# Optimization experiments

Hardware: AMD Instinct MI355X
Metric: run time of the kernel (lower is better)

## Reference

```python
import jax, jax.numpy as jnp
import numpy as np

N = 1500
GAT_IN = 32
GAT_OUT = 8
MLP_HIDDEN = 128
ALPHA = 0.2  # leaky relu slope
NEG_INF = -9.0e15


def setup_inputs() -> dict:
    key = jax.random.key(0)
    ks = jax.random.split(key, 16)
    eye = jnp.eye(N, dtype=jnp.float32)
    geo_adj = jnp.maximum((jax.random.uniform(ks[0], (N, N)) < 0.02).astype(jnp.float32), eye)
    sem_adj = jnp.maximum((jax.random.uniform(ks[1], (N, N)) < 0.02).astype(jnp.float32), eye)
    features = jax.random.normal(ks[2], (N, GAT_IN), dtype=jnp.float32)
    # all (i, j) region pairs, as in the original source
    ii, jj = jnp.meshgrid(jnp.arange(N), jnp.arange(N), indexing='ij')
    region_pairs = jnp.stack([ii.reshape(-1), jj.reshape(-1)], axis=1).astype(jnp.int64)
    distance_features = jax.random.uniform(ks[3], (N * N, 1), dtype=jnp.float32)
    def lin(k, fan_in, fan_out):
        return jax.random.normal(k, (fan_in, fan_out), dtype=jnp.float32) / jnp.sqrt(jnp.float32(fan_in))
    W0 = lin(ks[4], GAT_IN, GAT_OUT)
    W1 = lin(ks[5], GAT_OUT, GAT_OUT)
    W2 = lin(ks[6], GAT_OUT, GAT_OUT)
    a0 = lin(ks[7], 2 * GAT_OUT, 1)
    a1 = lin(ks[8], 2 * GAT_OUT, 1)
    a2 = lin(ks[9], 2 * GAT_OUT, 1)
    fc1_w = lin(ks[10], 2 * GAT_OUT + 1, MLP_HIDDEN)
    fc1_b = jnp.zeros((MLP_HIDDEN,), dtype=jnp.float32)
    fc2_w = lin(ks[11], MLP_HIDDEN, 1)
    fc2_b = jnp.zeros((1,), dtype=jnp.float32)
    return {"geo_adj": geo_adj, "sem_adj": sem_adj, "features": features,
            "region_pairs": region_pairs, "distance_features": distance_features,
            "W0": W0, "W1": W1, "W2": W2, "a0": a0, "a1": a1, "a2": a2,
            "fc1_w": fc1_w, "fc1_b": fc1_b, "fc2_w": fc2_w, "fc2_b": fc2_b}


def _gat_layer(combined_adj, feats, W, a):
    # h = W feats; attention score a([h_i || h_j]) decomposes into h_i@a1 + h_j@a2
    h = feats @ W                      # [N, out]
    f_src = h @ a[:GAT_OUT]            # [N, 1]
    f_dst = h @ a[GAT_OUT:]            # [N, 1]
    e = jax.nn.leaky_relu(f_src + f_dst.T, negative_slope=ALPHA)  # [N, N]
    e = e * combined_adj
    att = jax.nn.softmax(jnp.where(combined_adj > 0, e, NEG_INF), axis=1)
    return jax.nn.elu(att @ h)


def reference(geo_adj, sem_adj, features, region_pairs, distance_features,
              W0, W1, W2, a0, a1, a2, fc1_w, fc1_b, fc2_w, fc2_b):
    combined_adj = geo_adj + sem_adj
    enc = features
    for W, a in ((W0, a0), (W1, a1), (W2, a2)):
        enc = _gat_layer(combined_adj, enc, W, a)
    r1 = enc[region_pairs[:, 0]]       # [N^2, out]
    r2 = enc[region_pairs[:, 1]]       # [N^2, out]
    comb = jnp.concatenate([r1, r2, distance_features], axis=1)  # [N^2, 17]
    hid = jax.nn.relu(comb @ fc1_w + fc1_b)
    return hid @ fc2_w + fc2_b
```

## Files before the change

kernel.cpp:

```cpp
#include <hip/hip_runtime.h>
#include <hip/hip_bf16.h>

#define NN 1500
#define GIN 32
#define GOUT 8
#define HID 128
#define CAP 192

typedef float v2f __attribute__((ext_vector_type(2)));

__global__ void build_csr(const float* __restrict__ geo,
                          const float* __restrict__ sem,
                          int* __restrict__ csr_idx,
                          float* __restrict__ csr_val,
                          int* __restrict__ csr_cnt) {
    const int i = blockIdx.x;
    const int t = threadIdx.x;
    __shared__ int cnt;
    __shared__ int sidx[CAP];
    __shared__ float sval[CAP];
    if (t == 0) cnt = 0;
    __syncthreads();
    const float* grow = geo + (size_t)i * NN;
    const float* srow = sem + (size_t)i * NN;
    for (int q = t; q < NN / 4; q += 256) {
        float4 g = *(const float4*)(grow + 4 * q);
        float4 s = *(const float4*)(srow + 4 * q);
        float a[4] = {g.x + s.x, g.y + s.y, g.z + s.z, g.w + s.w};
        #pragma unroll
        for (int c = 0; c < 4; ++c) {
            if (a[c] > 0.f) {
                int p = atomicAdd(&cnt, 1);
                if (p < CAP) { sidx[p] = 4 * q + c; sval[p] = a[c]; }
            }
        }
    }
    __syncthreads();
    int c2 = cnt < CAP ? cnt : CAP;
    if (t == 0) csr_cnt[i] = c2;
    for (int p = t; p < c2; p += 256) {
        csr_idx[(size_t)i * CAP + p] = sidx[p];
        csr_val[(size_t)i * CAP + p] = sval[p];
    }
}

template<int IN>
__global__ void gat_layer(const float* __restrict__ enc,
                          const float* __restrict__ W,
                          const float* __restrict__ avec,
                          const int* __restrict__ csr_idx,
                          const float* __restrict__ csr_val,
                          const int* __restrict__ csr_cnt,
                          float* __restrict__ enc_out) {
    const int tid = threadIdx.x;
    const int lane = tid & 63;
    const int i = blockIdx.x * 4 + (tid >> 6);

    float hv = 0.f;
    if (lane < GOUT) {
        #pragma unroll 4
        for (int c = 0; c < IN; ++c)
            hv = fmaf(enc[(size_t)i * IN + c], W[c * GOUT + lane], hv);
    }
    float hi[GOUT];
    #pragma unroll
    for (int c = 0; c < GOUT; ++c) hi[c] = __shfl(hv, c, 64);
    float fsrc = 0.f;
    #pragma unroll
    for (int c = 0; c < GOUT; ++c) fsrc = fmaf(hi[c], avec[c], fsrc);

    const int cnt = csr_cnt[i];
    float den = 0.f;
    float num[GOUT] = {};
    for (int e = lane; e < cnt; e += 64) {
        int j = csr_idx[(size_t)i * CAP + e];
        float a = csr_val[(size_t)i * CAP + e];
        float hj[GOUT] = {};
        #pragma unroll
        for (int c4 = 0; c4 < IN / 4; ++c4) {
            float4 e4 = *(const float4*)(enc + (size_t)j * IN + 4 * c4);
            const float* ep = (const float*)&e4;
            #pragma unroll
            for (int c = 0; c < 4; ++c)
                #pragma unroll
                for (int k = 0; k < GOUT; ++k)
                    hj[k] = fmaf(ep[c], W[(4 * c4 + c) * GOUT + k], hj[k]);
        }
        float fd = 0.f;
        #pragma unroll
        for (int k = 0; k < GOUT; ++k) fd = fmaf(hj[k], avec[GOUT + k], fd);
        float ev = fsrc + fd;
        ev = (ev > 0.f) ? ev : 0.2f * ev;
        ev *= a;
        float p = __expf(ev);
        den += p;
        #pragma unroll
        for (int k = 0; k < GOUT; ++k) num[k] = fmaf(p, hj[k], num[k]);
    }
    #pragma unroll
    for (int off = 32; off > 0; off >>= 1) {
        den += __shfl_xor(den, off, 64);
        #pragma unroll
        for (int k = 0; k < GOUT; ++k) num[k] += __shfl_xor(num[k], off, 64);
    }
    if (lane < GOUT) {
        float v = num[lane] / den;
        enc_out[(size_t)i * GOUT + lane] = (v > 0.f) ? v : (__expf(v) - 1.f);
    }
}

#define TILE 48
#define STRIDE 132

__global__ __launch_bounds__(256, 3) void mlp_kernel(
        const float* __restrict__ enc,
        const float* __restrict__ dist,
        const float* __restrict__ fc1w,
        const float* __restrict__ fc1b,
        const float* __restrict__ fc2w,
        const float* __restrict__ fc2b,
        float* __restrict__ out) {
    __shared__ float Us[TILE * STRIDE];
    __shared__ float Vs[TILE * STRIDE];
    __shared__ float w16s[HID];
    __shared__ float f2s[HID];

    const int tid = threadIdx.x;
    const int i0 = blockIdx.y * TILE;
    const int j0 = blockIdx.x * TILE;

    {
        const int kg = tid & 31;
        const int k4 = kg << 2;
        const int rb = tid >> 5;
        float4 b4 = *(const float4*)(fc1b + k4);
        for (int r = rb; r < TILE; r += 8) {
            int gi = i0 + r; if (gi >= NN) gi = NN - 1;
            int gj = j0 + r; if (gj >= NN) gj = NN - 1;
            float4 u = b4;
            float4 v = {0.f, 0.f, 0.f, 0.f};
            #pragma unroll
            for (int c = 0; c < GOUT; ++c) {
                float ei = enc[(size_t)gi * GOUT + c];
                float ej = enc[(size_t)gj * GOUT + c];
                float4 wu = *(const float4*)(fc1w + c * HID + k4);
                float4 wv = *(const float4*)(fc1w + (GOUT + c) * HID + k4);
                u.x = fmaf(ei, wu.x, u.x); u.y = fmaf(ei, wu.y, u.y);
                u.z = fmaf(ei, wu.z, u.z); u.w = fmaf(ei, wu.w, u.w);
                v.x = fmaf(ej, wv.x, v.x); v.y = fmaf(ej, wv.y, v.y);
                v.z = fmaf(ej, wv.z, v.z); v.w = fmaf(ej, wv.w, v.w);
            }
            *(float4*)(Us + r * STRIDE + k4) = u;
            *(float4*)(Vs + r * STRIDE + k4) = v;
        }
        if (tid < HID) {
            w16s[tid] = fc1w[2 * GOUT * HID + tid];
            f2s[tid] = fc2w[tid];
        }
    }
    __syncthreads();

    const int tx = tid & 15;
    const int ty = tid >> 4;

    int irow[3], jcol[3];
    float d[3][3];
    #pragma unroll
    for (int ii = 0; ii < 3; ++ii) irow[ii] = i0 + ty + 16 * ii;
    #pragma unroll
    for (int jj = 0; jj < 3; ++jj) jcol[jj] = j0 + tx + 16 * jj;
    #pragma unroll
    for (int ii = 0; ii < 3; ++ii) {
        int ic = irow[ii] < NN ? irow[ii] : NN - 1;
        #pragma unroll
        for (int jj = 0; jj < 3; ++jj) {
            int jc = jcol[jj] < NN ? jcol[jj] : NN - 1;
            d[ii][jj] = dist[(size_t)ic * NN + jc];
        }
    }

    v2f acc[3][3] = {};
    for (int k = 0; k < HID; k += 4) {
        float4 u4[3], v4[3];
        #pragma unroll
        for (int ii = 0; ii < 3; ++ii)
            u4[ii] = *(const float4*)(Us + (ty + 16 * ii) * STRIDE + k);
        #pragma unroll
        for (int jj = 0; jj < 3; ++jj)
            v4[jj] = *(const float4*)(Vs + (tx + 16 * jj) * STRIDE + k);
        float4 wk = *(const float4*)(w16s + k);
        float4 fk = *(const float4*)(f2s + k);
        const v2f* wp = (const v2f*)&wk;
        const v2f* fp = (const v2f*)&fk;
        #pragma unroll
        for (int h = 0; h < 2; ++h) {
            v2f w2 = wp[h];
            v2f f2 = fp[h];
            #pragma unroll
            for (int ii = 0; ii < 3; ++ii) {
                v2f u2 = ((const v2f*)&u4[ii])[h];
                #pragma unroll
                for (int jj = 0; jj < 3; ++jj) {
                    v2f t = u2 + ((const v2f*)&v4[jj])[h];
                    t = t + w2 * d[ii][jj];
                    t = __builtin_elementwise_max(t, (v2f)0.f);
                    acc[ii][jj] = acc[ii][jj] + t * f2;
                }
            }
        }
    }

    const float b2 = fc2b[0];
    #pragma unroll
    for (int ii = 0; ii < 3; ++ii) {
        if (irow[ii] >= NN) continue;
        #pragma unroll
        for (int jj = 0; jj < 3; ++jj) {
            if (jcol[jj] >= NN) continue;
            out[(size_t)irow[ii] * NN + jcol[jj]] = acc[ii][jj].x + acc[ii][jj].y + b2;
        }
    }
}

extern "C" void kernel_launch(void* const* d_in, const int* in_sizes, int n_in,
                              void* d_out, int out_size, void* d_ws, size_t ws_size,
                              hipStream_t stream) {
    const float* geo  = (const float*)d_in[0];
    const float* sem  = (const float*)d_in[1];
    const float* feat = (const float*)d_in[2];
    const float* dist = (const float*)d_in[4];
    const float* W0   = (const float*)d_in[5];
    const float* W1   = (const float*)d_in[6];
    const float* W2   = (const float*)d_in[7];
    const float* a0   = (const float*)d_in[8];
    const float* a1   = (const float*)d_in[9];
    const float* a2   = (const float*)d_in[10];
    const float* fc1w = (const float*)d_in[11];
    const float* fc1b = (const float*)d_in[12];
    const float* fc2w = (const float*)d_in[13];
    const float* fc2b = (const float*)d_in[14];
    float* out = (float*)d_out;

    char* ws = (char*)d_ws;
    int*   csr_idx = (int*)ws;                         ws += sizeof(int) * NN * CAP;
    float* csr_val = (float*)ws;                       ws += sizeof(float) * NN * CAP;
    int*   csr_cnt = (int*)ws;                         ws += sizeof(int) * NN;
    float* encA    = (float*)ws;                       ws += sizeof(float) * NN * GOUT;
    float* encB    = (float*)ws;

    build_csr<<<NN, 256, 0, stream>>>(geo, sem, csr_idx, csr_val, csr_cnt);

    gat_layer<GIN><<<NN / 4, 256, 0, stream>>>(feat, W0, a0, csr_idx, csr_val, csr_cnt, encA);
    gat_layer<GOUT><<<NN / 4, 256, 0, stream>>>(encA, W1, a1, csr_idx, csr_val, csr_cnt, encB);
    gat_layer<GOUT><<<NN / 4, 256, 0, stream>>>(encB, W2, a2, csr_idx, csr_val, csr_cnt, encA);

    dim3 mg((NN + TILE - 1) / TILE, (NN + TILE - 1) / TILE);
    mlp_kernel<<<mg, 256, 0, stream>>>(encA, dist, fc1w, fc1b, fc2w, fc2b, out);
}
```

Before: 160.5 us.

## Fuse first GAT layer into CSR build and enlarge MLP register tile

The CSR-building kernel now also computes the first GAT layer, so one launch and a re-read of the CSR arrays go away. Each thread handles one neighbour and the result is reduced across the block. The pairwise MLP kernel moves from 48x48 tiles with 3x3 outputs per thread to 96x96 tiles with 6x6 outputs per thread. Its hidden dimension is staged through shared memory in two 64-wide phases, which raises register reuse of U/V loads but cuts occupancy to one block per SIMD-bound launch and gives only 256 blocks.

```diff
diff --git a/kernel.cpp b/kernel.cpp
--- a/kernel.cpp
+++ b/kernel.cpp
@@ -9,18 +9,25 @@
 
 typedef float v2f __attribute__((ext_vector_type(2)));
 
-__global__ void build_csr(const float* __restrict__ geo,
+__global__ void gat_first(const float* __restrict__ geo,
                           const float* __restrict__ sem,
+                          const float* __restrict__ feat,
+                          const float* __restrict__ W0,
+                          const float* __restrict__ a0,
                           int* __restrict__ csr_idx,
                           float* __restrict__ csr_val,
-                          int* __restrict__ csr_cnt) {
+                          int* __restrict__ csr_cnt,
+                          float* __restrict__ enc_out) {
     const int i = blockIdx.x;
     const int t = threadIdx.x;
     __shared__ int cnt;
     __shared__ int sidx[CAP];
     __shared__ float sval[CAP];
+    __shared__ float hi_s[GOUT];
+    __shared__ float wsum[4][GOUT + 1];
     if (t == 0) cnt = 0;
     __syncthreads();
+
     const float* grow = geo + (size_t)i * NN;
     const float* srow = sem + (size_t)i * NN;
     for (int q = t; q < NN / 4; q += 256) {
@@ -35,12 +42,68 @@
             }
         }
     }
+    if (t < GOUT) {
+        float hv = 0.f;
+        #pragma unroll 4
+        for (int c = 0; c < GIN; ++c)
+            hv = fmaf(feat[(size_t)i * GIN + c], W0[c * GOUT + t], hv);
+        hi_s[t] = hv;
+    }
     __syncthreads();
-    int c2 = cnt < CAP ? cnt : CAP;
+
+    const int c2 = cnt < CAP ? cnt : CAP;
     if (t == 0) csr_cnt[i] = c2;
     for (int p = t; p < c2; p += 256) {
         csr_idx[(size_t)i * CAP + p] = sidx[p];
         csr_val[(size_t)i * CAP + p] = sval[p];
+    }
+    float fsrc = 0.f;
+    #pragma unroll
+    for (int k = 0; k < GOUT; ++k) fsrc = fmaf(hi_s[k], a0[k], fsrc);
+
+    float den = 0.f;
+    float num[GOUT] = {};
+    if (t < c2) {
+        int j = sidx[t];
+        float a = sval[t];
+        float hj[GOUT] = {};
+        #pragma unroll
+        for (int c4 = 0; c4 < GIN / 4; ++c4) {
+            float4 e4 = *(const float4*)(feat + (size_t)j * GIN + 4 * c4);
+            const float* ep = (const float*)&e4;
+            #pragma unroll
+            for (int c = 0; c < 4; ++c)
+                #pragma unroll
+                for (int k = 0; k < GOUT; ++k)
+                    hj[k] = fmaf(ep[c], W0[(4 * c4 + c) * GOUT + k], hj[k]);
+        }
+        float fd = 0.f;
+        #pragma unroll
+        for (int k = 0; k < GOUT; ++k) fd = fmaf(hj[k], a0[GOUT + k], fd);
+        float ev = fsrc + fd;
+        ev = (ev > 0.f) ? ev : 0.2f * ev;
+        ev *= a;
+        float p = __expf(ev);
+        den = p;
+        #pragma unroll
+        for (int k = 0; k < GOUT; ++k) num[k] = p * hj[k];
+    }
+    #pragma unroll
+    for (int off = 32; off > 0; off >>= 1) {
+        den += __shfl_xor(den, off, 64);
+        #pragma unroll
+        for (int k = 0; k < GOUT; ++k) num[k] += __shfl_xor(num[k], off, 64);
+    }
+    if ((t & 63) == 0) {
+        wsum[t >> 6][0] = den;
+        #pragma unroll
+        for (int k = 0; k < GOUT; ++k) wsum[t >> 6][1 + k] = num[k];
+    }
+    __syncthreads();
+    if (t < GOUT) {
+        float L = wsum[0][0] + wsum[1][0] + wsum[2][0] + wsum[3][0];
+        float v = (wsum[0][1 + t] + wsum[1][1 + t] + wsum[2][1 + t] + wsum[3][1 + t]) / L;
+        enc_out[(size_t)i * GOUT + t] = (v > 0.f) ? v : (__expf(v) - 1.f);
     }
 }
 
@@ -109,10 +172,11 @@
     }
 }
 
-#define TILE 48
-#define STRIDE 132
-
-__global__ __launch_bounds__(256, 3) void mlp_kernel(
+#define MT 96
+#define KS 64
+#define KSTR 68
+
+__global__ __launch_bounds__(256, 1) void mlp_kernel(
         const float* __restrict__ enc,
         const float* __restrict__ dist,
         const float* __restrict__ fc1w,
@@ -120,102 +184,106 @@
         const float* __restrict__ fc2w,
         const float* __restrict__ fc2b,
         float* __restrict__ out) {
-    __shared__ float Us[TILE * STRIDE];
-    __shared__ float Vs[TILE * STRIDE];
+    __shared__ float Us[MT * KSTR];
+    __shared__ float Vs[MT * KSTR];
     __shared__ float w16s[HID];
     __shared__ float f2s[HID];
 
     const int tid = threadIdx.x;
-    const int i0 = blockIdx.y * TILE;
-    const int j0 = blockIdx.x * TILE;
-
-    {
-        const int kg = tid & 31;
-        const int k4 = kg << 2;
-        const int rb = tid >> 5;
-        float4 b4 = *(const float4*)(fc1b + k4);
-        for (int r = rb; r < TILE; r += 8) {
-            int gi = i0 + r; if (gi >= NN) gi = NN - 1;
-            int gj = j0 + r; if (gj >= NN) gj = NN - 1;
-            float4 u = b4;
-            float4 v = {0.f, 0.f, 0.f, 0.f};
-            #pragma unroll
-            for (int c = 0; c < GOUT; ++c) {
-                float ei = enc[(size_t)gi * GOUT + c];
-                float ej = enc[(size_t)gj * GOUT + c];
-                float4 wu = *(const float4*)(fc1w + c * HID + k4);
-                float4 wv = *(const float4*)(fc1w + (GOUT + c) * HID + k4);
-                u.x = fmaf(ei, wu.x, u.x); u.y = fmaf(ei, wu.y, u.y);
-                u.z = fmaf(ei, wu.z, u.z); u.w = fmaf(ei, wu.w, u.w);
-                v.x = fmaf(ej, wv.x, v.x); v.y = fmaf(ej, wv.y, v.y);
-                v.z = fmaf(ej, wv.z, v.z); v.w = fmaf(ej, wv.w, v.w);
-            }
-            *(float4*)(Us + r * STRIDE + k4) = u;
-            *(float4*)(Vs + r * STRIDE + k4) = v;
-        }
-        if (tid < HID) {
-            w16s[tid] = fc1w[2 * GOUT * HID + tid];
-            f2s[tid] = fc2w[tid];
-        }
-    }
-    __syncthreads();
-
+    const int i0 = blockIdx.y * MT;
+    const int j0 = blockIdx.x * MT;
     const int tx = tid & 15;
     const int ty = tid >> 4;
 
-    int irow[3], jcol[3];
-    float d[3][3];
-    #pragma unroll
-    for (int ii = 0; ii < 3; ++ii) irow[ii] = i0 + ty + 16 * ii;
-    #pragma unroll
-    for (int jj = 0; jj < 3; ++jj) jcol[jj] = j0 + tx + 16 * jj;
-    #pragma unroll
-    for (int ii = 0; ii < 3; ++ii) {
+    if (tid < HID) {
+        w16s[tid] = fc1w[2 * GOUT * HID + tid];
+        f2s[tid] = fc2w[tid];
+    }
+
+    int irow[6], jcol[6];
+    float d[6][6];
+    #pragma unroll
+    for (int ii = 0; ii < 6; ++ii) irow[ii] = i0 + ty + 16 * ii;
+    #pragma unroll
+    for (int jj = 0; jj < 6; ++jj) jcol[jj] = j0 + tx + 16 * jj;
+    #pragma unroll
+    for (int ii = 0; ii < 6; ++ii) {
         int ic = irow[ii] < NN ? irow[ii] : NN - 1;
         #pragma unroll
-        for (int jj = 0; jj < 3; ++jj) {
+        for (int jj = 0; jj < 6; ++jj) {
             int jc = jcol[jj] < NN ? jcol[jj] : NN - 1;
             d[ii][jj] = dist[(size_t)ic * NN + jc];
         }
     }
 
-    v2f acc[3][3] = {};
-    for (int k = 0; k < HID; k += 4) {
-        float4 u4[3], v4[3];
-        #pragma unroll
-        for (int ii = 0; ii < 3; ++ii)
-            u4[ii] = *(const float4*)(Us + (ty + 16 * ii) * STRIDE + k);
-        #pragma unroll
-        for (int jj = 0; jj < 3; ++jj)
-            v4[jj] = *(const float4*)(Vs + (tx + 16 * jj) * STRIDE + k);
-        float4 wk = *(const float4*)(w16s + k);
-        float4 fk = *(const float4*)(f2s + k);
-        const v2f* wp = (const v2f*)&wk;
-        const v2f* fp = (const v2f*)&fk;
-        #pragma unroll
-        for (int h = 0; h < 2; ++h) {
-            v2f w2 = wp[h];
-            v2f f2 = fp[h];
-            #pragma unroll
-            for (int ii = 0; ii < 3; ++ii) {
-                v2f u2 = ((const v2f*)&u4[ii])[h];
+    v2f acc[6][6] = {};
+
+    #pragma unroll
+    for (int ph = 0; ph < 2; ++ph) {
+        const int k0 = ph * KS;
+        for (int u = tid; u < 2 * MT * 16; u += 256) {
+            const int isU = (u < MT * 16);
+            const int q = isU ? u : u - MT * 16;
+            const int r = q >> 4;
+            const int k4 = k0 + ((q & 15) << 2);
+            int g = (isU ? i0 : j0) + r;
+            if (g >= NN) g = NN - 1;
+            float4 acc4;
+            if (isU) acc4 = *(const float4*)(fc1b + k4);
+            else acc4 = make_float4(0.f, 0.f, 0.f, 0.f);
+            const float* wbase = fc1w + (isU ? 0 : GOUT) * HID + k4;
+            const float* ep = enc + (size_t)g * GOUT;
+            #pragma unroll
+            for (int c = 0; c < GOUT; ++c) {
+                float e = ep[c];
+                float4 w4 = *(const float4*)(wbase + c * HID);
+                acc4.x = fmaf(e, w4.x, acc4.x);
+                acc4.y = fmaf(e, w4.y, acc4.y);
+                acc4.z = fmaf(e, w4.z, acc4.z);
+                acc4.w = fmaf(e, w4.w, acc4.w);
+            }
+            *(float4*)((isU ? Us : Vs) + r * KSTR + (k4 - k0)) = acc4;
+        }
+        __syncthreads();
+
+        for (int k4 = 0; k4 < KS; k4 += 4) {
+            float4 u4[6], v4[6];
+            #pragma unroll
+            for (int ii = 0; ii < 6; ++ii)
+                u4[ii] = *(const float4*)(Us + (ty + 16 * ii) * KSTR + k4);
+            #pragma unroll
+            for (int jj = 0; jj < 6; ++jj)
+                v4[jj] = *(const float4*)(Vs + (tx + 16 * jj) * KSTR + k4);
+            float4 wk = *(const float4*)(w16s + k0 + k4);
+            float4 fk = *(const float4*)(f2s + k0 + k4);
+            const v2f* wp = (const v2f*)&wk;
+            const v2f* fp = (const v2f*)&fk;
+            #pragma unroll
+            for (int h = 0; h < 2; ++h) {
+                v2f w2 = wp[h];
+                v2f f2 = fp[h];
                 #pragma unroll
-                for (int jj = 0; jj < 3; ++jj) {
-                    v2f t = u2 + ((const v2f*)&v4[jj])[h];
-                    t = t + w2 * d[ii][jj];
-                    t = __builtin_elementwise_max(t, (v2f)0.f);
-                    acc[ii][jj] = acc[ii][jj] + t * f2;
+                for (int ii = 0; ii < 6; ++ii) {
+                    v2f u2 = ((const v2f*)&u4[ii])[h];
+                    #pragma unroll
+                    for (int jj = 0; jj < 6; ++jj) {
+                        v2f tt = u2 + ((const v2f*)&v4[jj])[h];
+                        tt = tt + w2 * d[ii][jj];
+                        tt = __builtin_elementwise_max(tt, (v2f)0.f);
+                        acc[ii][jj] = acc[ii][jj] + tt * f2;
+                    }
                 }
             }
         }
+        __syncthreads();
     }
 
     const float b2 = fc2b[0];
     #pragma unroll
-    for (int ii = 0; ii < 3; ++ii) {
+    for (int ii = 0; ii < 6; ++ii) {
         if (irow[ii] >= NN) continue;
         #pragma unroll
-        for (int jj = 0; jj < 3; ++jj) {
+        for (int jj = 0; jj < 6; ++jj) {
             if (jcol[jj] >= NN) continue;
             out[(size_t)irow[ii] * NN + jcol[jj]] = acc[ii][jj].x + acc[ii][jj].y + b2;
         }
@@ -248,12 +316,11 @@
     float* encA    = (float*)ws;                       ws += sizeof(float) * NN * GOUT;
     float* encB    = (float*)ws;
 
-    build_csr<<<NN, 256, 0, stream>>>(geo, sem, csr_idx, csr_val, csr_cnt);
-
-    gat_layer<GIN><<<NN / 4, 256, 0, stream>>>(feat, W0, a0, csr_idx, csr_val, csr_cnt, encA);
+    gat_first<<<NN, 256, 0, stream>>>(geo, sem, feat, W0, a0,
+                                      csr_idx, csr_val, csr_cnt, encA);
     gat_layer<GOUT><<<NN / 4, 256, 0, stream>>>(encA, W1, a1, csr_idx, csr_val, csr_cnt, encB);
     gat_layer<GOUT><<<NN / 4, 256, 0, stream>>>(encB, W2, a2, csr_idx, csr_val, csr_cnt, encA);
 
-    dim3 mg((NN + TILE - 1) / TILE, (NN + TILE - 1) / TILE);
+    dim3 mg(16, 16);
     mlp_kernel<<<mg, 256, 0, stream>>>(encA, dist, fc1w, fc1b, fc2w, fc2b, out);
 }
```

Measured after the change: 166.3 us. 1.04x slower.
